# Optimization experiments

Hardware: AMD Instinct MI355X
Metric: run time of the kernel (lower is better)

## Reference

```python
import jax, jax.numpy as jnp
import numpy as np

D_MODEL = 1024
STATE = 16

def setup_inputs() -> dict:
    key = jax.random.key(0)
    ks = jax.random.split(key, 7)
    x = jax.random.normal(ks[0], (4, 4096, D_MODEL), dtype=jnp.float32)
    A_log = jax.random.normal(ks[1], (STATE,), dtype=jnp.float32)
    B = jax.random.normal(ks[2], (STATE, D_MODEL), dtype=jnp.float32) * 0.05
    C = jax.random.normal(ks[3], (D_MODEL, STATE), dtype=jnp.float32) * 0.05
    D = jax.random.normal(ks[4], (D_MODEL,), dtype=jnp.float32)
    W_delta = jax.random.normal(ks[5], (D_MODEL, D_MODEL), dtype=jnp.float32) * 0.02
    b_delta = jax.random.normal(ks[6], (D_MODEL,), dtype=jnp.float32) * 0.02
    return {"x": x, "A_log": A_log, "B": B, "C": C, "D": D,
            "W_delta": W_delta, "b_delta": b_delta}

def reference(x, A_log, B, C, D, W_delta, b_delta):
    # delta: softplus(Linear(x)).mean(-1) -> (b, l)
    delta = jax.nn.softplus(jnp.einsum('bld,ed->ble', x, W_delta) + b_delta).mean(-1)
    A = -jnp.exp(A_log)                         # (n,)
    Bx = jnp.einsum('bld,nd->bln', x, B)        # (b, l, n)
    dA = jnp.exp(delta[..., None] * A)          # (b, l, n)
    dBx = delta[..., None] * Bx                 # (b, l, n)

    def step(h, inp):
        dA_t, dBx_t = inp                       # (b, n) each
        h = dA_t * h + dBx_t
        return h, h

    h0 = jnp.zeros((x.shape[0], A_log.shape[0]), dtype=x.dtype)
    _, hs = jax.lax.scan(step, h0, (jnp.swapaxes(dA, 0, 1), jnp.swapaxes(dBx, 0, 1)))
    hs = jnp.swapaxes(hs, 0, 1)                 # (b, l, n)
    y = jnp.einsum('bln,dn->bld', hs, C) + D * x
    return y
```

## Files before the change

kernel.cpp:

```cpp
#include <hip/hip_runtime.h>
#include <hip/hip_bf16.h>
#include <stdint.h>

#define DM 1024
#define NS 16
#define LSEQ 4096
#define NB 4
#define MTOT (NB*LSEQ)
#define NC 128
#define LC 32

typedef __attribute__((ext_vector_type(8))) short bf16x8;
typedef __attribute__((ext_vector_type(4))) float f32x4;

__device__ __forceinline__ unsigned short f2bf(float f) {
    unsigned int u = __float_as_uint(f);
    unsigned int r = (u + 0x7FFFu + ((u >> 16) & 1u)) >> 16;
    return (unsigned short)r;
}

__device__ __forceinline__ float bf2f(unsigned short u) {
    return __uint_as_float(((unsigned int)u) << 16);
}

__device__ __forceinline__ float softplus_f(float v) {
    return v > 15.f ? v : __logf(1.f + __expf(v));
}

__device__ __forceinline__ void gload_lds16(const void* g, void* l) {
    __builtin_amdgcn_global_load_lds(
        (const __attribute__((address_space(1))) unsigned int*)g,
        (__attribute__((address_space(3))) unsigned int*)l, 16, 0, 0);
}

__global__ __launch_bounds__(256) void pre_kernel(
    const float4* __restrict__ x4, const float4* __restrict__ W4,
    const float4* __restrict__ B4, ushort4* __restrict__ xb4,
    ushort4* __restrict__ wb4, ushort4* __restrict__ bbf4,
    float* __restrict__ delta_raw)
{
    int bid = blockIdx.x, t = threadIdx.x;
    if (bid < 16384) {
        size_t i = (size_t)bid * 256 + t;
        float4 v = x4[i];
        ushort4 o; o.x = f2bf(v.x); o.y = f2bf(v.y); o.z = f2bf(v.z); o.w = f2bf(v.w);
        xb4[i] = o;
    } else if (bid < 17408) {
        int i = (bid - 16384) * 256 + t;
        float4 v = W4[i];
        ushort4 o; o.x = f2bf(v.x); o.y = f2bf(v.y); o.z = f2bf(v.z); o.w = f2bf(v.w);
        wb4[i] = o;
    } else if (bid < 17424) {
        int i = (bid - 17408) * 256 + t;
        float4 v = B4[i];
        ushort4 o; o.x = f2bf(v.x); o.y = f2bf(v.y); o.z = f2bf(v.z); o.w = f2bf(v.w);
        bbf4[i] = o;
    } else {
        int i = (bid - 17424) * 256 + t;
        ((float4*)delta_raw)[i] = (float4){0.f, 0.f, 0.f, 0.f};
    }
}

__global__ __launch_bounds__(256) void gemm_delta(
    const unsigned short* __restrict__ xb, const unsigned short* __restrict__ wb,
    const float* __restrict__ b_delta, float* __restrict__ delta_raw)
{
    __shared__ char lds[65536];
    int bid = blockIdx.x;
    int swz = (bid & 7) * 128 + (bid >> 3);
    int rb = swz >> 3, eb = swz & 7;
    int row0 = rb * 128, e0 = eb * 128;
    int tid = threadIdx.x;
    int lane = tid & 63, w = tid >> 6;
    int wr = w >> 1, wc = w & 1;
    int lm = lane & 15, lk = lane >> 4;

    int colsw = ((lane & 7) * 8) ^ ((lane >> 3) << 3);
    int rsub = lane >> 3;

    const unsigned short* pA[4];
    const unsigned short* pB[4];
    #pragma unroll
    for (int j = 0; j < 4; ++j) {
        int region = w * 4 + j;
        int r0 = region * 8 + rsub;
        pA[j] = xb + (size_t)(row0 + r0) * DM + colsw;
        pB[j] = wb + (size_t)(e0  + r0) * DM + colsw;
    }

    f32x4 acc[4][4];
    #pragma unroll
    for (int m = 0; m < 4; ++m)
        #pragma unroll
        for (int n = 0; n < 4; ++n)
            acc[m][n] = (f32x4){0.f, 0.f, 0.f, 0.f};

#define STAGE(BUF, KOFF) do { \
    _Pragma("unroll") \
    for (int j = 0; j < 4; ++j) { \
        int region = w * 4 + j; \
        gload_lds16(pA[j] + (KOFF), lds + (BUF) + region * 1024); \
        gload_lds16(pB[j] + (KOFF), lds + (BUF) + 16384 + region * 1024); \
    } } while (0)

#define COMPUTE(BUF) do { \
    __builtin_amdgcn_s_setprio(1); \
    _Pragma("unroll") \
    for (int kk = 0; kk < 2; ++kk) { \
        bf16x8 a[4], b[4]; \
        _Pragma("unroll") \
        for (int m = 0; m < 4; ++m) { \
            int r = wr * 64 + m * 16 + lm; \
            int cb = (kk * 64 + lk * 16) ^ ((r & 7) << 4); \
            a[m] = *(const bf16x8*)(lds + (BUF) + r * 128 + cb); \
        } \
        _Pragma("unroll") \
        for (int n = 0; n < 4; ++n) { \
            int r = wc * 64 + n * 16 + lm; \
            int cb = (kk * 64 + lk * 16) ^ ((r & 7) << 4); \
            b[n] = *(const bf16x8*)(lds + (BUF) + 16384 + r * 128 + cb); \
        } \
        _Pragma("unroll") \
        for (int m = 0; m < 4; ++m) \
            _Pragma("unroll") \
            for (int n = 0; n < 4; ++n) \
                acc[m][n] = __builtin_amdgcn_mfma_f32_16x16x32_bf16(a[m], b[n], acc[m][n], 0, 0, 0); \
    } \
    __builtin_amdgcn_s_setprio(0); \
} while (0)

#define KSTEP(CUR, NXT, KOFF) do { \
    STAGE(NXT, KOFF); \
    asm volatile("s_waitcnt vmcnt(8)\n\ts_barrier" ::: "memory"); \
    COMPUTE(CUR); \
    asm volatile("s_barrier" ::: "memory"); \
} while (0)

    STAGE(0, 0);
    int koff = 64;
    #pragma unroll 1
    for (int it = 0; it < 7; ++it) {
        KSTEP(0, 32768, koff);
        KSTEP(32768, 0, koff + 64);
        koff += 128;
    }
    KSTEP(0, 32768, 960);
    asm volatile("s_waitcnt vmcnt(0)\n\ts_barrier" ::: "memory");
    COMPUTE(32768);

#undef KSTEP
#undef COMPUTE
#undef STAGE

    float bd[4];
    #pragma unroll
    for (int n = 0; n < 4; ++n) bd[n] = b_delta[e0 + wc * 64 + n * 16 + lm];
    #pragma unroll
    for (int m = 0; m < 4; ++m) {
        #pragma unroll
        for (int r = 0; r < 4; ++r) {
            float s = 0.f;
            #pragma unroll
            for (int n = 0; n < 4; ++n) s += softplus_f(acc[m][n][r] + bd[n]);
            s += __shfl_xor(s, 1, 16);
            s += __shfl_xor(s, 2, 16);
            s += __shfl_xor(s, 4, 16);
            s += __shfl_xor(s, 8, 16);
            if (lm == 0) {
                int row = row0 + wr * 64 + m * 16 + lk * 4 + r;
                atomicAdd(&delta_raw[row], s);
            }
        }
    }
}

__global__ __launch_bounds__(256) void bx_mfma(
    const unsigned short* __restrict__ xb, const unsigned short* __restrict__ bbf,
    float* __restrict__ Bx)
{
    int tid = threadIdx.x, lane = tid & 63, w = tid >> 6;
    int rb = blockIdx.x * 4 + w;
    int r0 = rb * 16;
    int lm = lane & 15, lk = lane >> 4;
    const unsigned short* pa = xb + (size_t)(r0 + lm) * DM + lk * 8;
    const unsigned short* pb = bbf + (size_t)lm * DM + lk * 8;
    f32x4 acc = (f32x4){0.f, 0.f, 0.f, 0.f};
    #pragma unroll 4
    for (int k0 = 0; k0 < DM; k0 += 32) {
        bf16x8 a = *(const bf16x8*)(pa + k0);
        bf16x8 b = *(const bf16x8*)(pb + k0);
        acc = __builtin_amdgcn_mfma_f32_16x16x32_bf16(a, b, acc, 0, 0, 0);
    }
    #pragma unroll
    for (int r = 0; r < 4; ++r)
        Bx[(size_t)(r0 + lk * 4 + r) * NS + lm] = acc[r];
}

__global__ __launch_bounds__(64) void scan_pass1(
    const float* __restrict__ delta_raw, const float* __restrict__ Bx,
    const float* __restrict__ A_log, float* __restrict__ cP, float* __restrict__ cH)
{
    __shared__ float dl[LC];
    __shared__ float bxl[LC * NS];
    int bid = blockIdx.x;
    int b = bid >> 7, c = bid & 127;
    int l0 = c * LC;
    int t = threadIdx.x;
    size_t base = (size_t)b * LSEQ + l0;
    if (t < LC) dl[t] = delta_raw[base + t] * (1.f / 1024.f);
    const float4* src = (const float4*)(Bx + base * NS);
    float4* dst = (float4*)bxl;
    dst[t] = src[t];
    dst[t + 64] = src[t + 64];
    __syncthreads();
    if (t < NS) {
        float a = -__expf(A_log[t]);
        float P = 1.f, h = 0.f;
        #pragma unroll
        for (int s = 0; s < LC; ++s) {
            float dlt = dl[s];
            float dA = __expf(dlt * a);
            h = dA * h + dlt * bxl[s * NS + t];
            P *= dA;
        }
        int idx = (b * NC + c) * NS + t;
        cP[idx] = P; cH[idx] = h;
    }
}

__global__ __launch_bounds__(256) void y_kernel(
    const unsigned short* __restrict__ xb, const float* __restrict__ delta_raw,
    const float* __restrict__ Bx, const float* __restrict__ A_log,
    const float* __restrict__ cP, const float* __restrict__ cH,
    const float* __restrict__ C, const float* __restrict__ Dv, float* __restrict__ y)
{
    __shared__ float dl[LC];
    __shared__ float bxl[LC * NS];
    __shared__ float hsl[LC * NS];
    __shared__ float pbuf[NC * NS];
    __shared__ float hbuf[NC * NS];
    int bid = blockIdx.x;
    int b = bid >> 7, c = bid & 127;
    int l0 = c * LC;
    int t = threadIdx.x;
    size_t base = (size_t)b * LSEQ + l0;
    if (t < LC) dl[t] = delta_raw[base + t] * (1.f / 1024.f);
    if (t < 128) ((float4*)bxl)[t] = ((const float4*)(Bx + base * NS))[t];
    {
        const float4* p4 = (const float4*)(cP + (size_t)b * NC * NS);
        const float4* h4 = (const float4*)(cH + (size_t)b * NC * NS);
        ((float4*)pbuf)[t] = p4[t];         ((float4*)pbuf)[t + 256] = p4[t + 256];
        ((float4*)hbuf)[t] = h4[t];         ((float4*)hbuf)[t + 256] = h4[t + 256];
    }
    __syncthreads();
    if (t < NS) {
        float h = 0.f;
        for (int cc = 0; cc < c; ++cc) {
            int idx = cc * NS + t;
            h = pbuf[idx] * h + hbuf[idx];
        }
        float a = -__expf(A_log[t]);
        #pragma unroll
        for (int s = 0; s < LC; ++s) {
            float dlt = dl[s];
            float dA = __expf(dlt * a);
            h = dA * h + dlt * bxl[s * NS + t];
            hsl[s * NS + t] = h;
        }
    }
    __syncthreads();

    int d0 = t * 4;
    float cr[4][NS];
    #pragma unroll
    for (int dd = 0; dd < 4; ++dd)
        #pragma unroll
        for (int nn = 0; nn < 4; ++nn) {
            float4 c4 = ((const float4*)C)[((d0 + dd) * NS + nn * 4) >> 2];
            cr[dd][nn * 4 + 0] = c4.x; cr[dd][nn * 4 + 1] = c4.y;
            cr[dd][nn * 4 + 2] = c4.z; cr[dd][nn * 4 + 3] = c4.w;
        }
    float4 dv = ((const float4*)Dv)[t];
    const ushort4* xr = (const ushort4*)(xb + base * DM) + t;
    float4* yr = (float4*)(y + base * DM) + t;
    for (int s = 0; s < LC; ++s) {
        float hv[NS];
        #pragma unroll
        for (int n = 0; n < NS; ++n) hv[n] = hsl[s * NS + n];
        ushort4 xv4 = xr[s * 256];
        float4 o;
        o.x = dv.x * bf2f(xv4.x); o.y = dv.y * bf2f(xv4.y);
        o.z = dv.z * bf2f(xv4.z); o.w = dv.w * bf2f(xv4.w);
        #pragma unroll
        for (int n = 0; n < NS; ++n) {
            o.x += hv[n] * cr[0][n];
            o.y += hv[n] * cr[1][n];
            o.z += hv[n] * cr[2][n];
            o.w += hv[n] * cr[3][n];
        }
        yr[s * 256] = o;
    }
}

extern "C" void kernel_launch(void* const* d_in, const int* in_sizes, int n_in,
                              void* d_out, int out_size, void* d_ws, size_t ws_size,
                              hipStream_t stream)
{
    const float* x     = (const float*)d_in[0];
    const float* A_log = (const float*)d_in[1];
    const float* B     = (const float*)d_in[2];
    const float* C     = (const float*)d_in[3];
    const float* Dv    = (const float*)d_in[4];
    const float* Wd    = (const float*)d_in[5];
    const float* bd    = (const float*)d_in[6];
    float* y = (float*)d_out;

    char* ws = (char*)d_ws;
    unsigned short* xb = (unsigned short*)ws;
    unsigned short* wb = (unsigned short*)(ws + 33554432);
    float* delta_raw   = (float*)(ws + 35651584);
    float* Bx          = (float*)(ws + 35717120);
    float* cP          = (float*)(ws + 36765696);
    float* cH          = (float*)(ws + 36798464);
    unsigned short* bbf= (unsigned short*)(ws + 36831232);

    pre_kernel<<<17440, 256, 0, stream>>>((const float4*)x, (const float4*)Wd,
                                          (const float4*)B, (ushort4*)xb,
                                          (ushort4*)wb, (ushort4*)bbf, delta_raw);
    gemm_delta<<<1024, 256, 0, stream>>>(xb, wb, bd, delta_raw);
    bx_mfma<<<256, 256, 0, stream>>>(xb, bbf, Bx);
    scan_pass1<<<NB * NC, 64, 0, stream>>>(delta_raw, Bx, A_log, cP, cH);
    y_kernel<<<NB * NC, 256, 0, stream>>>(xb, delta_raw, Bx, A_log, cP, cH, C, Dv, y);
}
```

Before: 101.9 us.

## Enlarge delta GEMM tile to 256x256 with 512-thread blocks

Changes the delta projection GEMM from 128x128 tiles on 256-thread blocks to 256x256 tiles on 512-thread blocks, with 128 KB of double-buffered LDS. Each warp now computes a 128x64 sub-tile and keeps its B fragments in registers across the m loop. The aim is less global and LDS traffic per FLOP and a grid that fits one block per CU in a single wave. The cost is lower occupancy and higher register pressure per wave.

```diff
diff --git a/kernel.cpp b/kernel.cpp
--- a/kernel.cpp
+++ b/kernel.cpp
@@ -61,18 +61,18 @@
     }
 }
 
-__global__ __launch_bounds__(256) void gemm_delta(
+__global__ __launch_bounds__(512) void gemm_delta(
     const unsigned short* __restrict__ xb, const unsigned short* __restrict__ wb,
     const float* __restrict__ b_delta, float* __restrict__ delta_raw)
 {
-    __shared__ char lds[65536];
+    __shared__ char lds[131072];
     int bid = blockIdx.x;
-    int swz = (bid & 7) * 128 + (bid >> 3);
-    int rb = swz >> 3, eb = swz & 7;
-    int row0 = rb * 128, e0 = eb * 128;
+    int swz = (bid & 7) * 32 + (bid >> 3);
+    int mb = swz >> 2, nb = swz & 3;
+    int row0 = mb * 256, e0 = nb * 256;
     int tid = threadIdx.x;
     int lane = tid & 63, w = tid >> 6;
-    int wr = w >> 1, wc = w & 1;
+    int wr = w >> 2, wc = w & 3;
     int lm = lane & 15, lk = lane >> 4;
 
     int colsw = ((lane & 7) * 8) ^ ((lane >> 3) << 3);
@@ -88,9 +88,15 @@
         pB[j] = wb + (size_t)(e0  + r0) * DM + colsw;
     }
 
-    f32x4 acc[4][4];
-    #pragma unroll
-    for (int m = 0; m < 4; ++m)
+    int sterm = (lm & 7) << 4;
+    int off0 = (lk * 16) ^ sterm;
+    int off1 = (64 + lk * 16) ^ sterm;
+    int aBase = (wr * 128 + lm) * 128;
+    int bBase = 32768 + (wc * 64 + lm) * 128;
+
+    f32x4 acc[8][4];
+    #pragma unroll
+    for (int m = 0; m < 8; ++m)
         #pragma unroll
         for (int n = 0; n < 4; ++n)
             acc[m][n] = (f32x4){0.f, 0.f, 0.f, 0.f};
@@ -100,31 +106,26 @@
     for (int j = 0; j < 4; ++j) { \
         int region = w * 4 + j; \
         gload_lds16(pA[j] + (KOFF), lds + (BUF) + region * 1024); \
-        gload_lds16(pB[j] + (KOFF), lds + (BUF) + 16384 + region * 1024); \
+        gload_lds16(pB[j] + (KOFF), lds + (BUF) + 32768 + region * 1024); \
     } } while (0)
 
 #define COMPUTE(BUF) do { \
+    bf16x8 bq[4][2]; \
+    _Pragma("unroll") \
+    for (int n = 0; n < 4; ++n) { \
+        bq[n][0] = *(const bf16x8*)(lds + (BUF) + bBase + n * 2048 + off0); \
+        bq[n][1] = *(const bf16x8*)(lds + (BUF) + bBase + n * 2048 + off1); \
+    } \
     __builtin_amdgcn_s_setprio(1); \
     _Pragma("unroll") \
-    for (int kk = 0; kk < 2; ++kk) { \
-        bf16x8 a[4], b[4]; \
-        _Pragma("unroll") \
-        for (int m = 0; m < 4; ++m) { \
-            int r = wr * 64 + m * 16 + lm; \
-            int cb = (kk * 64 + lk * 16) ^ ((r & 7) << 4); \
-            a[m] = *(const bf16x8*)(lds + (BUF) + r * 128 + cb); \
-        } \
+    for (int m = 0; m < 8; ++m) { \
+        bf16x8 a0 = *(const bf16x8*)(lds + (BUF) + aBase + m * 2048 + off0); \
+        bf16x8 a1 = *(const bf16x8*)(lds + (BUF) + aBase + m * 2048 + off1); \
         _Pragma("unroll") \
         for (int n = 0; n < 4; ++n) { \
-            int r = wc * 64 + n * 16 + lm; \
-            int cb = (kk * 64 + lk * 16) ^ ((r & 7) << 4); \
-            b[n] = *(const bf16x8*)(lds + (BUF) + 16384 + r * 128 + cb); \
+            acc[m][n] = __builtin_amdgcn_mfma_f32_16x16x32_bf16(a0, bq[n][0], acc[m][n], 0, 0, 0); \
+            acc[m][n] = __builtin_amdgcn_mfma_f32_16x16x32_bf16(a1, bq[n][1], acc[m][n], 0, 0, 0); \
         } \
-        _Pragma("unroll") \
-        for (int m = 0; m < 4; ++m) \
-            _Pragma("unroll") \
-            for (int n = 0; n < 4; ++n) \
-                acc[m][n] = __builtin_amdgcn_mfma_f32_16x16x32_bf16(a[m], b[n], acc[m][n], 0, 0, 0); \
     } \
     __builtin_amdgcn_s_setprio(0); \
 } while (0)
@@ -140,13 +141,13 @@
     int koff = 64;
     #pragma unroll 1
     for (int it = 0; it < 7; ++it) {
-        KSTEP(0, 32768, koff);
-        KSTEP(32768, 0, koff + 64);
+        KSTEP(0, 65536, koff);
+        KSTEP(65536, 0, koff + 64);
         koff += 128;
     }
-    KSTEP(0, 32768, 960);
+    KSTEP(0, 65536, 960);
     asm volatile("s_waitcnt vmcnt(0)\n\ts_barrier" ::: "memory");
-    COMPUTE(32768);
+    COMPUTE(65536);
 
 #undef KSTEP
 #undef COMPUTE
@@ -156,7 +157,7 @@
     #pragma unroll
     for (int n = 0; n < 4; ++n) bd[n] = b_delta[e0 + wc * 64 + n * 16 + lm];
     #pragma unroll
-    for (int m = 0; m < 4; ++m) {
+    for (int m = 0; m < 8; ++m) {
         #pragma unroll
         for (int r = 0; r < 4; ++r) {
             float s = 0.f;
@@ -167,7 +168,7 @@
             s += __shfl_xor(s, 4, 16);
             s += __shfl_xor(s, 8, 16);
             if (lm == 0) {
-                int row = row0 + wr * 64 + m * 16 + lk * 4 + r;
+                int row = row0 + wr * 128 + m * 16 + lk * 4 + r;
                 atomicAdd(&delta_raw[row], s);
             }
         }
@@ -327,7 +328,7 @@
     pre_kernel<<<17440, 256, 0, stream>>>((const float4*)x, (const float4*)Wd,
                                           (const float4*)B, (ushort4*)xb,
                                           (ushort4*)wb, (ushort4*)bbf, delta_raw);
-    gemm_delta<<<1024, 256, 0, stream>>>(xb, wb, bd, delta_raw);
+    gemm_delta<<<256, 512, 0, stream>>>(xb, wb, bd, delta_raw);
     bx_mfma<<<256, 256, 0, stream>>>(xb, bbf, Bx);
     scan_pass1<<<NB * NC, 64, 0, stream>>>(delta_raw, Bx, A_log, cP, cH);
     y_kernel<<<NB * NC, 256, 0, stream>>>(xb, delta_raw, Bx, A_log, cP, cH, C, Dv, y);
```

After: 97.97 us. 3.9% less time.
